# Kernel tuning notes

Hardware: AMD Instinct MI355X
Metric: run time of the kernel (lower is better)

Reference implementation:

```python
import jax, jax.numpy as jnp
import numpy as np

NUM_HEADS = 8
NEG_SLOPE = 0.2


def setup_inputs() -> dict:
    key = jax.random.key(0)
    k1, k2, k3, k4 = jax.random.split(key, 4)
    B, N, D_IN, D_K, D_V = 4, 4096, 256, 256, 256
    x = jax.random.normal(k1, (B, N, D_IN), dtype=jnp.float32)
    Wq = jax.random.normal(k2, (D_IN, D_K), dtype=jnp.float32) * (1.0 / np.sqrt(D_IN))
    Wk = jax.random.normal(k3, (D_IN, D_K), dtype=jnp.float32) * (1.0 / np.sqrt(D_IN))
    Wv = jax.random.normal(k4, (D_IN, D_V), dtype=jnp.float32) * (1.0 / np.sqrt(D_IN))
    return {"x": x, "Wq": Wq, "Wk": Wk, "Wv": Wv}


def reference(x, Wq, Wk, Wv):
    B, N, _ = x.shape
    nh = NUM_HEADS
    dim_k = Wq.shape[1]
    dim_v = Wv.shape[1]
    dk, dv = dim_k // nh, dim_v // nh
    nor_fact = 1.0 / np.sqrt(dk)
    # project and split heads: [B, H, N, dk]
    q = (x @ Wq).reshape(B, N, nh, dk).transpose(0, 2, 1, 3)
    k = (x @ Wk).reshape(B, N, nh, dk).transpose(0, 2, 1, 3)
    v = (x @ Wv).reshape(B, N, nh, dv).transpose(0, 2, 1, 3)
    # all-pairs scores, scaled then LeakyReLU (no softmax)
    dist = jnp.einsum('bhnd,bhmd->bhnm', q, k) * nor_fact
    dist = jnp.where(dist >= 0, dist, NEG_SLOPE * dist)
    att = jnp.einsum('bhnm,bhmd->bhnd', dist, v)
    return att.transpose(0, 2, 1, 3).reshape(B, N, dim_v)
```

## Files before the change

### kernel.cpp

```cpp
#include <hip/hip_runtime.h>

typedef __attribute__((ext_vector_type(8))) short short8;
typedef __attribute__((ext_vector_type(4))) short short4v;
typedef __attribute__((ext_vector_type(4))) float f32x4;
typedef __attribute__((ext_vector_type(2))) unsigned int u32x2;

#define MFMA16x32(A, B, C) \
  __builtin_amdgcn_mfma_f32_16x16x32_bf16((A), (B), (C), 0, 0, 0)

#if defined(__has_builtin)
#if __has_builtin(__builtin_amdgcn_mfma_f32_16x16x16bf16_1k)
#define HAVE_MFMA_1K 1
#endif
#endif

__device__ __forceinline__ f32x4 mfma16x16(short4v a, short4v b, f32x4 c) {
#ifdef HAVE_MFMA_1K
  return __builtin_amdgcn_mfma_f32_16x16x16bf16_1k(a, b, c, 0, 0, 0);
#else
  f32x4 d;
  asm("v_mfma_f32_16x16x16_bf16 %0, %1, %2, %3"
      : "=v"(d)
      : "v"(a), "v"(b), "v"(c));
  return d;
#endif
}

__device__ __forceinline__ void async_cp16(const unsigned short* g, void* l) {
  __builtin_amdgcn_global_load_lds(
      (const __attribute__((address_space(1))) unsigned int*)g,
      (__attribute__((address_space(3))) unsigned int*)l, 16, 0, 0);
}

__device__ __forceinline__ unsigned int fbits(float f) {
  return __builtin_bit_cast(unsigned int, f);
}
__device__ __forceinline__ unsigned int pack_bf16(float a, float b) {
  return __builtin_amdgcn_perm(fbits(b), fbits(a), 0x07060302u);
}
__device__ __forceinline__ unsigned short bf16_rne(float f) {
  unsigned int u = fbits(f);
  return (unsigned short)((u + 0x8000u) >> 16);
}

__global__ __launch_bounds__(256) void xconv_kernel(
    const float* __restrict__ x, unsigned short* __restrict__ xb) {
  const size_t i = ((size_t)blockIdx.x * 256 + threadIdx.x) * 4;
  const float4 f = *(const float4*)(x + i);
  u32x2 u = {(unsigned int)bf16_rne(f.x) | ((unsigned int)bf16_rne(f.y) << 16),
             (unsigned int)bf16_rne(f.z) | ((unsigned int)bf16_rne(f.w) << 16)};
  *(u32x2*)(xb + i) = u;
}

__global__ __launch_bounds__(256) void wtrans_kernel(
    const float* __restrict__ Wq, const float* __restrict__ Wk,
    const float* __restrict__ Wv, unsigned short* __restrict__ WT) {
  __shared__ float tile[32][33];
  const int bid = blockIdx.x;
  const int g = bid / 64, rem = bid % 64;
  const int k0 = (rem >> 3) * 32, n0 = (rem & 7) * 32;
  const float* W = (g == 0) ? Wq : (g == 1) ? Wk : Wv;
  const int t = threadIdx.x;
  {
    const int kr = t >> 3, nc = (t & 7) * 4;
    const float4 f = *(const float4*)(W + (size_t)(k0 + kr) * 256 + n0 + nc);
    tile[kr][nc + 0] = f.x; tile[kr][nc + 1] = f.y;
    tile[kr][nc + 2] = f.z; tile[kr][nc + 3] = f.w;
  }
  __syncthreads();
  {
    const int nr = t >> 3, kc = (t & 7) * 4;
    unsigned int u0 = (unsigned int)bf16_rne(tile[kc + 0][nr]) |
                      ((unsigned int)bf16_rne(tile[kc + 1][nr]) << 16);
    unsigned int u1 = (unsigned int)bf16_rne(tile[kc + 2][nr]) |
                      ((unsigned int)bf16_rne(tile[kc + 3][nr]) << 16);
    u32x2 u = {u0, u1};
    *(u32x2*)(WT + (size_t)g * 65536 + (size_t)(n0 + nr) * 256 + k0 + kc) = u;
  }
}

__global__ __launch_bounds__(256, 2) void proj_kernel(
    const unsigned short* __restrict__ xb, const unsigned short* __restrict__ WT,
    unsigned short* __restrict__ QH, unsigned short* __restrict__ KH,
    unsigned short* __restrict__ VT) {
  __shared__ __align__(16) char smem[65536];
  const int tid = threadIdx.x;
  const int w = tid >> 6, lane = tid & 63, l15 = lane & 15, quad = lane >> 4;
  const int bid = blockIdx.x;
  const int mtile = bid / 6, nt = bid % 6;
  const int g = nt >> 1, n0 = (nt & 1) * 128;
  const int m0 = mtile * 128;

  const int srow = lane >> 3, useg = lane & 7;
  const int swz = (useg ^ srow) * 8;
  const unsigned short* aS = xb + (size_t)(m0 + w * 32 + srow) * 256 + swz;
  const unsigned short* bS =
      WT + (size_t)g * 65536 + (size_t)(n0 + w * 32 + srow) * 256 + swz;

#pragma unroll
  for (int j = 0; j < 4; j++) {
    async_cp16(aS + j * 2048, smem + w * 4096 + j * 1024);
    async_cp16(bS + j * 2048, smem + 16384 + w * 4096 + j * 1024);
  }
  __syncthreads();

  const f32x4 zero = {0.f, 0.f, 0.f, 0.f};
  f32x4 acc[2][8];
#pragma unroll
  for (int s = 0; s < 2; s++)
#pragma unroll
    for (int c = 0; c < 8; c++) acc[s][c] = zero;

  const int sw = l15 & 7;
  for (int t = 0; t < 4; t++) {
    const int nb = t & 1;
    const int kn = ((t + 1) & 3) * 64;
#pragma unroll
    for (int j = 0; j < 4; j++) {
      async_cp16(aS + kn + j * 2048,
                 smem + (nb ^ 1) * 32768 + w * 4096 + j * 1024);
      async_cp16(bS + kn + j * 2048,
                 smem + (nb ^ 1) * 32768 + 16384 + w * 4096 + j * 1024);
    }
    const char* Ab = smem + nb * 32768;
    const char* Bb = Ab + 16384;
#pragma unroll
    for (int ks = 0; ks < 2; ks++) {
      const int seg = ((ks * 4 + quad) ^ sw) * 16;
      short8 af[2], bf[8];
#pragma unroll
      for (int s = 0; s < 2; s++)
        af[s] = *(const short8*)(Ab + (w * 32 + s * 16 + l15) * 128 + seg);
#pragma unroll
      for (int c = 0; c < 8; c++)
        bf[c] = *(const short8*)(Bb + (c * 16 + l15) * 128 + seg);
      if (g < 2) {
#pragma unroll
        for (int s = 0; s < 2; s++)
#pragma unroll
          for (int c = 0; c < 8; c++)
            acc[s][c] = MFMA16x32(bf[c], af[s], acc[s][c]);
      } else {
#pragma unroll
        for (int s = 0; s < 2; s++)
#pragma unroll
          for (int c = 0; c < 8; c++)
            acc[s][c] = MFMA16x32(af[s], bf[c], acc[s][c]);
      }
    }
    __syncthreads();
  }

  if (g < 2) {
    unsigned short* O = g ? KH : QH;
    const float sc = g ? 1.0f : 0.17677669529663688f;
#pragma unroll
    for (int s = 0; s < 2; s++)
#pragma unroll
      for (int c = 0; c < 8; c++) {
        const int row = m0 + w * 32 + s * 16 + l15;
        const int col = n0 + c * 16 + quad * 4;
        const int bb = row >> 12, nn = row & 4095;
        const int hh = col >> 5, dl = col & 31;
        u32x2 pk = {pack_bf16(acc[s][c][0] * sc, acc[s][c][1] * sc),
                    pack_bf16(acc[s][c][2] * sc, acc[s][c][3] * sc)};
        *(u32x2*)(O + ((size_t)(bb * 8 + hh) * 4096 + nn) * 32 + dl) = pk;
      }
  } else {
#pragma unroll
    for (int s = 0; s < 2; s++)
#pragma unroll
      for (int c = 0; c < 8; c++) {
        const int col = n0 + c * 16 + l15;
        const int hh = col >> 5, dl = col & 31;
        const int row = m0 + w * 32 + s * 16 + quad * 4;
        const int bb = row >> 12, nn = row & 4095;
        u32x2 pk = {pack_bf16(acc[s][c][0], acc[s][c][1]),
                    pack_bf16(acc[s][c][2], acc[s][c][3])};
        *(u32x2*)(VT + (size_t)((bb * 8 + hh) * 32 + dl) * 4096 + nn) = pk;
      }
  }
}

__global__ __launch_bounds__(512, 2) void attn_kernel(
    const unsigned short* __restrict__ QH, const unsigned short* __restrict__ KH,
    const unsigned short* __restrict__ VT, float* __restrict__ out) {
  __shared__ __align__(16) char smem[16384];
  const int tid = threadIdx.x;
  const int w = tid >> 6, lane = tid & 63, l15 = lane & 15, quad = lane >> 4;
  const int bid = blockIdx.x;
  const int bh = bid & 31, qh = bid >> 5;
  const int b = bh >> 3, h = bh & 7;
  const int qbase = qh * 512 + w * 64;

  const unsigned short* Qp =
      QH + ((size_t)bh * 4096 + qbase + l15) * 32 + quad * 8;
  short8 qf[4];
#pragma unroll
  for (int s = 0; s < 4; s++) qf[s] = *(const short8*)(Qp + (size_t)s * 512);

  const bool isK = (w < 4);
  const unsigned short* src0;
  int kstr, wbOff;
  if (isK) {
    const int key = w * 16 + (lane >> 2), dseg = lane & 3;
    src0 = KH + ((size_t)bh * 4096 + key) * 32 + dseg * 8;
    kstr = 32;
    wbOff = w * 1024;
  } else {
    const int r = (w - 4) * 8 + (lane >> 3), useg = lane & 7;
    src0 = VT + ((size_t)bh * 32 + r) * 4096 + ((useg ^ (r & 7)) * 8);
    kstr = 1;
    wbOff = 4096 + (w - 4) * 1024;
  }

  async_cp16(src0, smem + wbOff);
  __syncthreads();

  const f32x4 zero = {0.f, 0.f, 0.f, 0.f};
  f32x4 acc[4][2];
#pragma unroll
  for (int s = 0; s < 4; s++) {
    acc[s][0] = zero;
    acc[s][1] = zero;
  }

  const int rs = l15 & 7;
  for (int i = 0; i < 64; i++) {
    const int nb = i & 1;
    const int kn = ((i + 1) & 63) * 64;
    async_cp16(src0 + (size_t)kn * kstr, smem + (nb ^ 1) * 8192 + wbOff);

    const char* Kb = smem + nb * 8192;
    const char* Vb = Kb + 4096;
    short8 kf[4];
#pragma unroll
    for (int c = 0; c < 4; c++)
      kf[c] = *(const short8*)(Kb + (c * 16 + l15) * 64 + quad * 16);
    short4v vf[2][4];
#pragma unroll
    for (int dt = 0; dt < 2; dt++) {
      const char* Vr = Vb + (dt * 16 + l15) * 128 + (quad & 1) * 8;
#pragma unroll
      for (int c = 0; c < 4; c++) {
        const int tt = c * 2 + (quad >> 1);
        vf[dt][c] = *(const short4v*)(Vr + ((tt ^ rs) * 16));
      }
    }

#pragma unroll
    for (int s = 0; s < 4; s++) {
#pragma unroll
      for (int c = 0; c < 4; c++) {
        f32x4 st = MFMA16x32(kf[c], qf[s], zero);
        float t0 = fmaxf(st[0], 0.2f * st[0]);
        float t1 = fmaxf(st[1], 0.2f * st[1]);
        float t2 = fmaxf(st[2], 0.2f * st[2]);
        float t3 = fmaxf(st[3], 0.2f * st[3]);
        u32x2 pk = {pack_bf16(t0, t1), pack_bf16(t2, t3)};
        const short4v pb = __builtin_bit_cast(short4v, pk);
#pragma unroll
        for (int dt = 0; dt < 2; dt++)
          acc[s][dt] = mfma16x16(vf[dt][c], pb, acc[s][dt]);
      }
    }
    __syncthreads();
  }

#pragma unroll
  for (int s = 0; s < 4; s++)
#pragma unroll
    for (int dt = 0; dt < 2; dt++)
      *(f32x4*)(out + ((size_t)b * 4096 + qbase + s * 16 + l15) * 256 + h * 32 +
                dt * 16 + quad * 4) = acc[s][dt];
}

extern "C" void kernel_launch(void* const* d_in, const int* in_sizes, int n_in,
                              void* d_out, int out_size, void* d_ws,
                              size_t ws_size, hipStream_t stream) {
  const float* x = (const float*)d_in[0];
  const float* Wq = (const float*)d_in[1];
  const float* Wk = (const float*)d_in[2];
  const float* Wv = (const float*)d_in[3];
  float* out = (float*)d_out;

  unsigned short* ws = (unsigned short*)d_ws;
  unsigned short* QHb = ws;
  unsigned short* KHb = ws + 4194304;
  unsigned short* VTb = ws + 2 * 4194304;
  unsigned short* xbb = ws + 3 * 4194304;
  unsigned short* WTb = ws + 4 * 4194304;

  xconv_kernel<<<4096, 256, 0, stream>>>(x, xbb);
  wtrans_kernel<<<192, 256, 0, stream>>>(Wq, Wk, Wv, WTb);
  proj_kernel<<<768, 256, 0, stream>>>(xbb, WTb, QHb, KHb, VTb);
  attn_kernel<<<256, 512, 0, stream>>>(QHb, KHb, VTb, out);
}
```

Baseline: 174.8 us.

## Switch attention to 32x32 MFMA tiles, merge prep kernels, precompute projection offsets

The attention kernel now uses 32x32x16 bf16 MFMA for the scores and 32x32x8 for the value product. It runs 256-thread blocks that own 256 queries each, every wave loads both K and V slices, and the K-loop is unrolled by two with fixed buffer indices. The x conversion and weight transpose kernels are merged into one launch. The projection kernel precomputes its per-row source pointers and LDS offsets and fully unrolls its k-loop. The larger MFMA shapes are meant to cut instruction count and improve operand reuse, at the cost of higher register pressure and a new fragment layout.

```diff
diff --git a/kernel.cpp b/kernel.cpp
--- a/kernel.cpp
+++ b/kernel.cpp
@@ -3,23 +3,25 @@
 typedef __attribute__((ext_vector_type(8))) short short8;
 typedef __attribute__((ext_vector_type(4))) short short4v;
 typedef __attribute__((ext_vector_type(4))) float f32x4;
+typedef __attribute__((ext_vector_type(16))) float f32x16;
 typedef __attribute__((ext_vector_type(2))) unsigned int u32x2;
 
 #define MFMA16x32(A, B, C) \
   __builtin_amdgcn_mfma_f32_16x16x32_bf16((A), (B), (C), 0, 0, 0)
+#define MFMA32x16(A, B, C) \
+  __builtin_amdgcn_mfma_f32_32x32x16_bf16((A), (B), (C), 0, 0, 0)
 
 #if defined(__has_builtin)
-#if __has_builtin(__builtin_amdgcn_mfma_f32_16x16x16bf16_1k)
-#define HAVE_MFMA_1K 1
+#if __has_builtin(__builtin_amdgcn_mfma_f32_32x32x8bf16_1k)
+#define HAVE_32X8 1
 #endif
 #endif
-
-__device__ __forceinline__ f32x4 mfma16x16(short4v a, short4v b, f32x4 c) {
-#ifdef HAVE_MFMA_1K
-  return __builtin_amdgcn_mfma_f32_16x16x16bf16_1k(a, b, c, 0, 0, 0);
+__device__ __forceinline__ f32x16 mfma32x8(short4v a, short4v b, f32x16 c) {
+#ifdef HAVE_32X8
+  return __builtin_amdgcn_mfma_f32_32x32x8bf16_1k(a, b, c, 0, 0, 0);
 #else
-  f32x4 d;
-  asm("v_mfma_f32_16x16x16_bf16 %0, %1, %2, %3"
+  f32x16 d;
+  asm("v_mfma_f32_32x32x8_bf16 %0, %1, %2, %3"
       : "=v"(d)
       : "v"(a), "v"(b), "v"(c));
   return d;
@@ -42,22 +44,25 @@
   unsigned int u = fbits(f);
   return (unsigned short)((u + 0x8000u) >> 16);
 }
-
-__global__ __launch_bounds__(256) void xconv_kernel(
-    const float* __restrict__ x, unsigned short* __restrict__ xb) {
-  const size_t i = ((size_t)blockIdx.x * 256 + threadIdx.x) * 4;
-  const float4 f = *(const float4*)(x + i);
-  u32x2 u = {(unsigned int)bf16_rne(f.x) | ((unsigned int)bf16_rne(f.y) << 16),
-             (unsigned int)bf16_rne(f.z) | ((unsigned int)bf16_rne(f.w) << 16)};
-  *(u32x2*)(xb + i) = u;
-}
-
-__global__ __launch_bounds__(256) void wtrans_kernel(
-    const float* __restrict__ Wq, const float* __restrict__ Wk,
-    const float* __restrict__ Wv, unsigned short* __restrict__ WT) {
+__device__ __forceinline__ float lk(float x) { return fmaxf(x, 0.2f * x); }
+
+__global__ __launch_bounds__(256) void prep_kernel(
+    const float* __restrict__ x, const float* __restrict__ Wq,
+    const float* __restrict__ Wk, const float* __restrict__ Wv,
+    unsigned short* __restrict__ xb, unsigned short* __restrict__ WT) {
+  const int bid = blockIdx.x;
+  if (bid < 4096) {
+    const size_t i = ((size_t)bid * 256 + threadIdx.x) * 4;
+    const float4 f = *(const float4*)(x + i);
+    u32x2 u = {
+        (unsigned int)bf16_rne(f.x) | ((unsigned int)bf16_rne(f.y) << 16),
+        (unsigned int)bf16_rne(f.z) | ((unsigned int)bf16_rne(f.w) << 16)};
+    *(u32x2*)(xb + i) = u;
+    return;
+  }
   __shared__ float tile[32][33];
-  const int bid = blockIdx.x;
-  const int g = bid / 64, rem = bid % 64;
+  const int wb = bid - 4096;
+  const int g = wb / 64, rem = wb % 64;
   const int k0 = (rem >> 3) * 32, n0 = (rem & 7) * 32;
   const float* W = (g == 0) ? Wq : (g == 1) ? Wk : Wv;
   const int t = threadIdx.x;
@@ -93,14 +98,19 @@
 
   const int srow = lane >> 3, useg = lane & 7;
   const int swz = (useg ^ srow) * 8;
-  const unsigned short* aS = xb + (size_t)(m0 + w * 32 + srow) * 256 + swz;
-  const unsigned short* bS =
-      WT + (size_t)g * 65536 + (size_t)(n0 + w * 32 + srow) * 256 + swz;
-
+  const unsigned short* aSj[4];
+  const unsigned short* bSj[4];
 #pragma unroll
   for (int j = 0; j < 4; j++) {
-    async_cp16(aS + j * 2048, smem + w * 4096 + j * 1024);
-    async_cp16(bS + j * 2048, smem + 16384 + w * 4096 + j * 1024);
+    aSj[j] = xb + (size_t)(m0 + w * 32 + j * 8 + srow) * 256 + swz;
+    bSj[j] = WT + (size_t)g * 65536 +
+             (size_t)(n0 + w * 32 + j * 8 + srow) * 256 + swz;
+  }
+
+#pragma unroll
+  for (int j = 0; j < 4; j++) {
+    async_cp16(aSj[j], smem + w * 4096 + j * 1024);
+    async_cp16(bSj[j], smem + 16384 + w * 4096 + j * 1024);
   }
   __syncthreads();
 
@@ -111,29 +121,33 @@
 #pragma unroll
     for (int c = 0; c < 8; c++) acc[s][c] = zero;
 
-  const int sw = l15 & 7;
+  const int sega = ((quad) ^ (l15 & 7)) * 16;
+  int aoff[2], boff[8];
+#pragma unroll
+  for (int s = 0; s < 2; s++) aoff[s] = (w * 32 + s * 16 + l15) * 128;
+#pragma unroll
+  for (int c = 0; c < 8; c++) boff[c] = 16384 + (c * 16 + l15) * 128;
+
+#pragma unroll
   for (int t = 0; t < 4; t++) {
     const int nb = t & 1;
     const int kn = ((t + 1) & 3) * 64;
 #pragma unroll
     for (int j = 0; j < 4; j++) {
-      async_cp16(aS + kn + j * 2048,
-                 smem + (nb ^ 1) * 32768 + w * 4096 + j * 1024);
-      async_cp16(bS + kn + j * 2048,
+      async_cp16(aSj[j] + kn, smem + (nb ^ 1) * 32768 + w * 4096 + j * 1024);
+      async_cp16(bSj[j] + kn,
                  smem + (nb ^ 1) * 32768 + 16384 + w * 4096 + j * 1024);
     }
-    const char* Ab = smem + nb * 32768;
-    const char* Bb = Ab + 16384;
 #pragma unroll
     for (int ks = 0; ks < 2; ks++) {
-      const int seg = ((ks * 4 + quad) ^ sw) * 16;
+      const int sg = ks ? (sega ^ 64) : sega;
       short8 af[2], bf[8];
 #pragma unroll
       for (int s = 0; s < 2; s++)
-        af[s] = *(const short8*)(Ab + (w * 32 + s * 16 + l15) * 128 + seg);
+        af[s] = *(const short8*)(smem + nb * 32768 + aoff[s] + sg);
 #pragma unroll
       for (int c = 0; c < 8; c++)
-        bf[c] = *(const short8*)(Bb + (c * 16 + l15) * 128 + seg);
+        bf[c] = *(const short8*)(smem + nb * 32768 + boff[c] + sg);
       if (g < 2) {
 #pragma unroll
         for (int s = 0; s < 2; s++)
@@ -182,97 +196,92 @@
   }
 }
 
-__global__ __launch_bounds__(512, 2) void attn_kernel(
+__global__ __launch_bounds__(256, 2) void attn_kernel(
     const unsigned short* __restrict__ QH, const unsigned short* __restrict__ KH,
     const unsigned short* __restrict__ VT, float* __restrict__ out) {
   __shared__ __align__(16) char smem[16384];
   const int tid = threadIdx.x;
-  const int w = tid >> 6, lane = tid & 63, l15 = lane & 15, quad = lane >> 4;
+  const int w = tid >> 6, lane = tid & 63, l31 = lane & 31, half = lane >> 5;
   const int bid = blockIdx.x;
-  const int bh = bid & 31, qh = bid >> 5;
+  const int bh = bid & 31, qt = bid >> 5;
   const int b = bh >> 3, h = bh & 7;
-  const int qbase = qh * 512 + w * 64;
-
-  const unsigned short* Qp =
-      QH + ((size_t)bh * 4096 + qbase + l15) * 32 + quad * 8;
-  short8 qf[4];
-#pragma unroll
-  for (int s = 0; s < 4; s++) qf[s] = *(const short8*)(Qp + (size_t)s * 512);
-
-  const bool isK = (w < 4);
-  const unsigned short* src0;
-  int kstr, wbOff;
-  if (isK) {
-    const int key = w * 16 + (lane >> 2), dseg = lane & 3;
-    src0 = KH + ((size_t)bh * 4096 + key) * 32 + dseg * 8;
-    kstr = 32;
-    wbOff = w * 1024;
-  } else {
-    const int r = (w - 4) * 8 + (lane >> 3), useg = lane & 7;
-    src0 = VT + ((size_t)bh * 32 + r) * 4096 + ((useg ^ (r & 7)) * 8);
-    kstr = 1;
-    wbOff = 4096 + (w - 4) * 1024;
-  }
-
-  async_cp16(src0, smem + wbOff);
+  const int qbase = qt * 256 + w * 64;
+
+  const unsigned short* Qp = QH + ((size_t)bh * 4096 + qbase + l31) * 32 + half * 8;
+  short8 qf[2][2];
+#pragma unroll
+  for (int qg = 0; qg < 2; qg++)
+#pragma unroll
+    for (int kh = 0; kh < 2; kh++)
+      qf[qg][kh] = *(const short8*)(Qp + qg * 1024 + kh * 16);
+
+  const unsigned short* gK =
+      KH + ((size_t)bh * 4096 + w * 16 + (lane >> 2)) * 32 + (lane & 3) * 8;
+  const int vd = w * 8 + (lane >> 3);
+  const unsigned short* gV =
+      VT + ((size_t)bh * 32 + vd) * 4096 + ((lane & 7) ^ (vd & 7)) * 8;
+
+  const int kbase = l31 * 64 + half * 16;
+  int voff[8];
+#pragma unroll
+  for (int kk = 0; kk < 8; kk++)
+    voff[kk] = 4096 + l31 * 128 + ((kk ^ (l31 & 7)) * 16) + half * 8;
+
+  async_cp16(gK, smem + w * 1024);
+  async_cp16(gV, smem + 4096 + w * 1024);
+  gK += 2048;
+  gV += 64;
   __syncthreads();
 
-  const f32x4 zero = {0.f, 0.f, 0.f, 0.f};
-  f32x4 acc[4][2];
-#pragma unroll
-  for (int s = 0; s < 4; s++) {
-    acc[s][0] = zero;
-    acc[s][1] = zero;
-  }
-
-  const int rs = l15 & 7;
-  for (int i = 0; i < 64; i++) {
-    const int nb = i & 1;
-    const int kn = ((i + 1) & 63) * 64;
-    async_cp16(src0 + (size_t)kn * kstr, smem + (nb ^ 1) * 8192 + wbOff);
-
-    const char* Kb = smem + nb * 8192;
-    const char* Vb = Kb + 4096;
-    short8 kf[4];
-#pragma unroll
-    for (int c = 0; c < 4; c++)
-      kf[c] = *(const short8*)(Kb + (c * 16 + l15) * 64 + quad * 16);
-    short4v vf[2][4];
-#pragma unroll
-    for (int dt = 0; dt < 2; dt++) {
-      const char* Vr = Vb + (dt * 16 + l15) * 128 + (quad & 1) * 8;
-#pragma unroll
-      for (int c = 0; c < 4; c++) {
-        const int tt = c * 2 + (quad >> 1);
-        vf[dt][c] = *(const short4v*)(Vr + ((tt ^ rs) * 16));
-      }
+  f32x16 z16;
+  f32x16 acc[2];
+#pragma unroll
+  for (int i = 0; i < 16; i++) { z16[i] = 0.f; acc[0][i] = 0.f; acc[1][i] = 0.f; }
+
+#define ATTN_BODY(B_)                                                         \
+  {                                                                           \
+    async_cp16(gK, smem + ((B_) ^ 1) * 8192 + w * 1024);                      \
+    async_cp16(gV, smem + ((B_) ^ 1) * 8192 + 4096 + w * 1024);               \
+    gK += 2048;                                                               \
+    gV += 64;                                                                 \
+    short8 kf[2][2];                                                          \
+    _Pragma("unroll") for (int kt = 0; kt < 2; kt++)                          \
+        _Pragma("unroll") for (int kh = 0; kh < 2; kh++) kf[kt][kh] =         \
+        *(const short8*)(smem + (B_)*8192 + kbase + kt * 2048 + kh * 32);     \
+    short4v vf[8];                                                            \
+    _Pragma("unroll") for (int kk = 0; kk < 8; kk++) vf[kk] =                 \
+        *(const short4v*)(smem + (B_)*8192 + voff[kk]);                       \
+    _Pragma("unroll") for (int qg = 0; qg < 2; qg++) {                        \
+      _Pragma("unroll") for (int kt = 0; kt < 2; kt++) {                      \
+        f32x16 st = MFMA32x16(kf[kt][0], qf[qg][0], z16);                     \
+        st = MFMA32x16(kf[kt][1], qf[qg][1], st);                             \
+        _Pragma("unroll") for (int g = 0; g < 4; g++) {                       \
+          u32x2 pk = {pack_bf16(lk(st[4 * g + 0]), lk(st[4 * g + 1])),        \
+                      pack_bf16(lk(st[4 * g + 2]), lk(st[4 * g + 3]))};       \
+          acc[qg] =                                                           \
+              mfma32x8(vf[kt * 4 + g], __builtin_bit_cast(short4v, pk),       \
+                       acc[qg]);                                              \
+        }                                                                     \
+      }                                                                       \
+    }                                                                         \
+    __syncthreads();                                                          \
+  }
+
+  for (int it = 0; it < 64; it += 2) {
+    ATTN_BODY(0)
+    ATTN_BODY(1)
+  }
+#undef ATTN_BODY
+
+#pragma unroll
+  for (int qg = 0; qg < 2; qg++)
+#pragma unroll
+    for (int g = 0; g < 4; g++) {
+      f32x4 o = {acc[qg][4 * g + 0], acc[qg][4 * g + 1], acc[qg][4 * g + 2],
+                 acc[qg][4 * g + 3]};
+      *(f32x4*)(out + ((size_t)b * 4096 + qbase + qg * 32 + l31) * 256 +
+                h * 32 + g * 8 + half * 4) = o;
     }
-
-#pragma unroll
-    for (int s = 0; s < 4; s++) {
-#pragma unroll
-      for (int c = 0; c < 4; c++) {
-        f32x4 st = MFMA16x32(kf[c], qf[s], zero);
-        float t0 = fmaxf(st[0], 0.2f * st[0]);
-        float t1 = fmaxf(st[1], 0.2f * st[1]);
-        float t2 = fmaxf(st[2], 0.2f * st[2]);
-        float t3 = fmaxf(st[3], 0.2f * st[3]);
-        u32x2 pk = {pack_bf16(t0, t1), pack_bf16(t2, t3)};
-        const short4v pb = __builtin_bit_cast(short4v, pk);
-#pragma unroll
-        for (int dt = 0; dt < 2; dt++)
-          acc[s][dt] = mfma16x16(vf[dt][c], pb, acc[s][dt]);
-      }
-    }
-    __syncthreads();
-  }
-
-#pragma unroll
-  for (int s = 0; s < 4; s++)
-#pragma unroll
-    for (int dt = 0; dt < 2; dt++)
-      *(f32x4*)(out + ((size_t)b * 4096 + qbase + s * 16 + l15) * 256 + h * 32 +
-                dt * 16 + quad * 4) = acc[s][dt];
 }
 
 extern "C" void kernel_launch(void* const* d_in, const int* in_sizes, int n_in,
@@ -291,8 +300,7 @@
   unsigned short* xbb = ws + 3 * 4194304;
   unsigned short* WTb = ws + 4 * 4194304;
 
-  xconv_kernel<<<4096, 256, 0, stream>>>(x, xbb);
-  wtrans_kernel<<<192, 256, 0, stream>>>(Wq, Wk, Wv, WTb);
+  prep_kernel<<<4288, 256, 0, stream>>>(x, Wq, Wk, Wv, xbb, WTb);
   proj_kernel<<<768, 256, 0, stream>>>(xbb, WTb, QHb, KHb, VTb);
-  attn_kernel<<<256, 512, 0, stream>>>(QHb, KHb, VTb, out);
-}
+  attn_kernel<<<512, 256, 0, stream>>>(QHb, KHb, VTb, out);
+}
```

After: 186.6 us. +6.7%, slower.
